# Optimization experiments

Hardware: AMD Instinct MI355X
Metric: run time of the kernel (lower is better)

Reference implementation:

```python
import jax, jax.numpy as jnp
import numpy as np

N_QUBITS = 10
Q_DEPTH = 6
MAX_LAYERS = 15
DIM = 2 ** N_QUBITS
INV_SQRT2 = 0.7071067811865476

# PennyLane ordering: wire 0 is the most-significant bit of the state index.
# All gates (H, RY, CNOT) are real, so the state stays real float32.

def _split(state, wire):
    a = 2 ** wire
    b = 2 ** (N_QUBITS - wire - 1)
    return state.reshape(-1, a, 2, b)

def apply_h(state, wire):
    s = _split(state, wire)
    s0, s1 = s[:, :, 0], s[:, :, 1]
    out = jnp.stack([(s0 + s1) * INV_SQRT2, (s0 - s1) * INV_SQRT2], axis=2)
    return out.reshape(-1, DIM)

def apply_ry(state, theta, wire):
    # theta: scalar (shared weight) or (B,) per-sample angle
    c = jnp.cos(theta * 0.5).reshape(-1, 1, 1)
    sn = jnp.sin(theta * 0.5).reshape(-1, 1, 1)
    s = _split(state, wire)
    s0, s1 = s[:, :, 0], s[:, :, 1]
    out = jnp.stack([c * s0 - sn * s1, sn * s0 + c * s1], axis=2)
    return out.reshape(-1, DIM)

def apply_cnot(state, ctrl):
    # CNOT on adjacent wires [ctrl, ctrl+1]
    a = 2 ** ctrl
    b = 2 ** (N_QUBITS - ctrl - 2)
    s = state.reshape(-1, a, 2, 2, b)
    out = jnp.stack([s[:, :, 0], s[:, :, 1, ::-1]], axis=2)
    return out.reshape(-1, DIM)

def expval_z(state):
    # <Z_j> = P(qubit j = 0) - P(qubit j = 1)
    zs = []
    for w in range(N_QUBITS):
        s = _split(state, w)
        p = s * s
        zs.append(jnp.sum(p[:, :, 0], axis=(1, 2)) - jnp.sum(p[:, :, 1], axis=(1, 2)))
    return jnp.stack(zs, axis=1)  # (B, n_qubits)

def simulate(q_in, q_params):
    B = q_in.shape[0]
    qw = q_params.reshape(MAX_LAYERS, N_QUBITS)
    state = jnp.zeros((B, DIM), q_in.dtype).at[:, 0].set(1.0)
    for w in range(N_QUBITS):
        state = apply_h(state, w)
    for w in range(N_QUBITS):
        state = apply_ry(state, q_in[:, w], w)
    for k in range(Q_DEPTH):
        for i in range(0, N_QUBITS - 1, 2):
            state = apply_cnot(state, i)
        for i in range(1, N_QUBITS - 1, 2):
            state = apply_cnot(state, i)
        for w in range(N_QUBITS):
            state = apply_ry(state, qw[k + 1, w], w)
    return expval_z(state)

def setup_inputs() -> dict:
    key = jax.random.key(0)
    k1, k2, k3, k4, k5 = jax.random.split(key, 5)
    B, D_IN, N_CLASSES = 8192, 512, 2
    return {
        "input_features": jax.random.normal(k1, (B, D_IN), jnp.float32),
        "W_red": jax.random.normal(k2, (N_QUBITS, D_IN), jnp.float32) * 0.04,
        "b_red": jnp.zeros((N_QUBITS,), jnp.float32),
        "q_params": 0.01 * jax.random.normal(k3, (MAX_LAYERS * N_QUBITS,), jnp.float32),
        "W_post": jax.random.normal(k4, (N_CLASSES, N_QUBITS), jnp.float32) * 0.3,
        "b_post": jax.random.normal(k5, (N_CLASSES,), jnp.float32) * 0.01,
    }

def reference(input_features, W_red, b_red, q_params, W_post, b_post):
    pre_out = input_features @ W_red.T + b_red           # (B, n_qubits)
    q_in = jnp.tanh(pre_out) * (np.pi / 2.0)             # angles in (-pi/2, pi/2)
    q_out = simulate(q_in, q_params)                     # (B, n_qubits) PauliZ expvals
    return q_out @ W_post.T + b_post                     # (B, n_classes)
```

## Files before the change

kernel.cpp:

```cpp
#include <hip/hip_runtime.h>
#include <math.h>

#define QDEPTH 6

typedef _Float16 h2 __attribute__((ext_vector_type(2)));

__device__ __forceinline__ int   h2i(h2 v)  { return __builtin_bit_cast(int, v); }
__device__ __forceinline__ h2    ih2(int v) { return __builtin_bit_cast(h2, v); }
__device__ __forceinline__ unsigned h2u(h2 v) { return __builtin_bit_cast(unsigned, v); }

__device__ __forceinline__ h2 cvt_pk(float a, float b) {
  return __builtin_bit_cast(h2, __builtin_amdgcn_cvt_pkrtz(a, b));
}

__device__ __forceinline__ h2 bper(int addr, h2 v) {
  return ih2(__builtin_amdgcn_ds_bpermute(addr, h2i(v)));
}

template<int CTRL>
__device__ __forceinline__ h2 dpph(h2 v) {
  int i = h2i(v);
  return ih2(__builtin_amdgcn_update_dpp(i, i, CTRL, 0xF, 0xF, true));
}

template<int CTRL>
__device__ __forceinline__ float dpp_add0(float v) {
  int i = __float_as_int(v);
  int r = __builtin_amdgcn_update_dpp(0, i, CTRL, 0xF, 0xF, false);
  return v + __int_as_float(r);
}

__device__ __forceinline__ float wave_sum(float v) {
  v = dpp_add0<0x111>(v);
  v = dpp_add0<0x112>(v);
  v = dpp_add0<0x114>(v);
  v = dpp_add0<0x118>(v);
  v = dpp_add0<0x142>(v);
  v = dpp_add0<0x143>(v);
  return v;
}

__device__ __forceinline__ float bcast63(float v) {
  return __int_as_float(__builtin_amdgcn_readlane(__float_as_int(v), 63));
}

__device__ __forceinline__ void pl32s(int& a, int& b) {
  asm("v_permlane32_swap_b32 %0, %1" : "+v"(a), "+v"(b));
}
__device__ __forceinline__ void pl16s(int& a, int& b) {
  asm("v_permlane16_swap_b32 %0, %1" : "+v"(a), "+v"(b));
}

__global__ void __launch_bounds__(256) qnet_kernel(
    const float* __restrict__ inp,
    const float* __restrict__ Wred,
    const float* __restrict__ bred,
    const float* __restrict__ qp,
    const float* __restrict__ Wpost,
    const float* __restrict__ bpost,
    float* __restrict__ out,
    int B) {
  __shared__ unsigned sco[QDEPTH * 29];
  {
    int t = threadIdx.x;
    if (t < 60) {
      int k = t / 10, w = t % 10;
      float ang = qp[(k + 1) * 10 + w] * 0.5f;
      float c = __cosf(ang), s = __sinf(ang);
      _Float16 ch = (_Float16)c, sh = (_Float16)s, nh = (_Float16)(-s);
      if (w < 9) {
        sco[k * 29 + w * 3 + 0] = h2u((h2){ch, ch});
        sco[k * 29 + w * 3 + 1] = h2u((h2){sh, sh});
        sco[k * 29 + w * 3 + 2] = h2u((h2){nh, nh});
      } else {
        sco[k * 29 + 27] = h2u((h2){ch, ch});
        sco[k * 29 + 28] = h2u((h2){nh, sh});
      }
    }
  }
  __syncthreads();

  int tid  = blockIdx.x * 256 + threadIdx.x;
  int wv   = tid >> 6;
  int lane = tid & 63;

  int o = lane ^ (((lane >> 4) & 1) << 3) ^ (((lane >> 2) & 1) << 1);
  int psrc = o ^ (((o >> 5) & 1) << 4) ^ (((o >> 3) & 1) << 2) ^ ((o >> 1) & 1);
  int addrP  = psrc << 2;
  int addrX4 = (lane ^ 4) << 2;
  bool cb1 = lane & 1;

  const float4* rA = (const float4*)(inp + (size_t)(2 * wv) * 512);
  const float4* rB = (const float4*)(inp + (size_t)(2 * wv + 1) * 512);
  float4 A0 = rA[lane], A1 = rA[lane + 64];
  float4 B0 = rB[lane], B1 = rB[lane + 64];
  float thA[10], thB[10];
#pragma unroll
  for (int q = 0; q < 10; ++q) {
    const float4* w4 = (const float4*)(Wred + q * 512);
    float4 w0 = w4[lane], w1 = w4[lane + 64];
    thA[q] = A0.x * w0.x + A0.y * w0.y + A0.z * w0.z + A0.w * w0.w
           + A1.x * w1.x + A1.y * w1.y + A1.z * w1.z + A1.w * w1.w;
    thB[q] = B0.x * w0.x + B0.y * w0.y + B0.z * w0.z + B0.w * w0.w
           + B1.x * w1.x + B1.y * w1.y + B1.z * w1.z + B1.w * w1.w;
  }

  h2 x[16];

#pragma unroll
  for (int e = 0; e < 2; ++e) {
    float g0[10], g1[10];
#pragma unroll
    for (int q = 0; q < 10; ++q) {
      float tot = bcast63(wave_sum(e ? thB[q] : thA[q])) + bred[q];
      float xc = fminf(fmaxf(tot, -15.f), 15.f);
      float u = __expf(2.f * xc);
      float tanhv = (u - 1.f) * __builtin_amdgcn_rcpf(u + 1.f);
      float t = tanhv * 0.78539816339744831f;
      float c = __cosf(t), s = __sinf(t);
      g0[q] = (c - s) * 0.70710678118654752f;
      g1[q] = (c + s) * 0.70710678118654752f;
    }
    float lf = 1.f;
#pragma unroll
    for (int w = 0; w < 6; ++w)
      lf *= ((lane >> (5 - w)) & 1) ? g1[w] : g0[w];
    float f67v[4];
#pragma unroll
    for (int j = 0; j < 4; ++j)
      f67v[j] = ((j & 2) ? g1[6] : g0[6]) * ((j & 1) ? g1[7] : g0[7]);
    float F89x[2], F89y[2];
    F89x[0] = g0[8] * g0[9]; F89y[0] = g0[8] * g1[9];
    F89x[1] = g1[8] * g0[9]; F89y[1] = g1[8] * g1[9];
#pragma unroll
    for (int i = 0; i < 8; ++i) {
      float m = lf * f67v[i >> 1];
      x[e * 8 + i] = cvt_pk(m * F89x[i & 1], m * F89y[i & 1]);
    }
  }

#pragma unroll
  for (int k = 0; k < QDEPTH; ++k) {
    const unsigned* L = sco + k * 29;

#pragma unroll
    for (int i = 0; i < 16; ++i) x[i] = bper(addrP, x[i]);
#pragma unroll
    for (int e = 0; e < 16; e += 8) {
      h2 t = x[e + 4]; x[e + 4] = x[e + 6]; x[e + 6] = t;
      t = x[e + 5]; x[e + 5] = x[e + 7]; x[e + 7] = t;
    }
#pragma unroll
    for (int e = 0; e < 16; e += 8) {
      h2 t = x[e + 2]; x[e + 2] = x[e + 3]; x[e + 3] = t;
      t = x[e + 6]; x[e + 6] = x[e + 7]; x[e + 7] = t;
    }

    { h2 cc9 = ih2(L[27]), ms9 = ih2(L[28]);
#pragma unroll
      for (int i = 0; i < 16; ++i) {
        h2 t = __builtin_shufflevector(x[i], x[i], 1, 0);
        int m = i & 7;
        bool flg = (m == 1 || m == 2 || m == 5 || m == 6);
        x[i] = flg ? (h2)(t * cc9 + x[i] * ms9) : (h2)(x[i] * cc9 + t * ms9);
      } }

    { h2 cc6 = ih2(L[18]), ss6 = ih2(L[19]), ns6 = ih2(L[20]);
      h2 AA = cb1 ? ns6 : cc6;
      h2 BB = cb1 ? cc6 : ns6;
      h2 CC = cb1 ? cc6 : ss6;
      h2 DD = cb1 ? ss6 : cc6;
#pragma unroll
      for (int i = 0; i < 16; ++i) if (!(i & 4)) {
        h2 u = x[i], w = x[i + 4];
        x[i]     = u * AA + w * BB;
        x[i + 4] = u * CC + w * DD;
      } }
    { h2 cc7 = ih2(L[21]), ss7 = ih2(L[22]), ns7 = ih2(L[23]);
#pragma unroll
      for (int i = 0; i < 16; ++i) if (!(i & 2)) {
        h2 u = x[i], w = x[i | 2];
        x[i]     = u * cc7 + w * ns7;
        x[i | 2] = w * cc7 + u * ss7;
      } }
    { h2 cc8 = ih2(L[24]), ss8 = ih2(L[25]), ns8 = ih2(L[26]);
#pragma unroll
      for (int i = 0; i < 16; ++i) if (!(i & 1)) {
        h2 u = x[i], w = x[i | 1];
        x[i]     = u * cc8 + w * ns8;
        x[i | 1] = w * cc8 + u * ss8;
      } }

    { h2 cc0 = ih2(L[0]), ss0 = ih2(L[1]), ns0 = ih2(L[2]);
#pragma unroll
      for (int j = 0; j < 8; ++j) {
        int a = h2i(x[2 * j]), b = h2i(x[2 * j + 1]);
        pl32s(a, b);
        h2 u = ih2(a), v = ih2(b);
        h2 nu = u * cc0 + v * ns0;
        h2 nv = v * cc0 + u * ss0;
        int na = h2i(nu), nb = h2i(nv);
        pl32s(na, nb);
        x[2 * j] = ih2(na); x[2 * j + 1] = ih2(nb);
      } }
    { h2 cc1 = ih2(L[3]), ss1 = ih2(L[4]), ns1 = ih2(L[5]);
#pragma unroll
      for (int j = 0; j < 8; ++j) {
        int a = h2i(x[2 * j]), b = h2i(x[2 * j + 1]);
        pl16s(a, b);
        h2 u = ih2(a), v = ih2(b);
        h2 nu = u * cc1 + v * ns1;
        h2 nv = v * cc1 + u * ss1;
        int na = h2i(nu), nb = h2i(nv);
        pl16s(na, nb);
        x[2 * j] = ih2(na); x[2 * j + 1] = ih2(nb);
      } }
    { h2 cc2 = ih2(L[6]), ss2 = ih2(L[7]), ns2 = ih2(L[8]);
      h2 gg = (lane & 8) ? ss2 : ns2;
#pragma unroll
      for (int i = 0; i < 16; ++i) {
        h2 p = dpph<0x128>(x[i]);
        x[i] = x[i] * cc2 + p * gg;
      } }
    { h2 cc3 = ih2(L[9]), ss3 = ih2(L[10]), ns3 = ih2(L[11]);
      h2 gg = (lane & 4) ? ss3 : ns3;
#pragma unroll
      for (int i = 0; i < 16; ++i) {
        h2 p = bper(addrX4, x[i]);
        x[i] = x[i] * cc3 + p * gg;
      } }
    { h2 cc4 = ih2(L[12]), ss4 = ih2(L[13]), ns4 = ih2(L[14]);
      h2 gg = (lane & 2) ? ss4 : ns4;
#pragma unroll
      for (int i = 0; i < 16; ++i) {
        h2 p = dpph<0x4E>(x[i]);
        x[i] = x[i] * cc4 + p * gg;
      } }
    { h2 cc5 = ih2(L[15]), ss5 = ih2(L[16]), ns5 = ih2(L[17]);
      h2 gg = (lane & 1) ? ss5 : ns5;
#pragma unroll
      for (int i = 0; i < 16; ++i) {
        h2 p = dpph<0xB1>(x[i]);
        x[i] = x[i] * cc5 + p * gg;
      } }
  }

  float A0w = 0.f, A1w = 0.f;
#pragma unroll
  for (int w = 0; w < 6; ++w) {
    bool b = (lane >> (5 - w)) & 1;
    A0w += b ? -Wpost[w] : Wpost[w];
    A1w += b ? -Wpost[10 + w] : Wpost[10 + w];
  }
  float oo[4];
#pragma unroll
  for (int e = 0; e < 2; ++e) {
    float q[8], d9 = 0.f;
#pragma unroll
    for (int i = 0; i < 8; ++i) {
      float lo = (float)x[e * 8 + i].x, hi = (float)x[e * 8 + i].y;
      float a2 = lo * lo, b2 = hi * hi;
      q[i] = a2 + b2;
      d9 += a2 - b2;
    }
    float A = q[0] + q[1], Bq = q[2] + q[3], C = q[4] + q[5], D = q[6] + q[7];
    float S  = (A + Bq) + (C + D);
    float z6 = (A + Bq) - (C + D);
    float z7 = (A - Bq) + (C - D);
    float E = q[0] - q[1], F = q[2] - q[3], G = q[4] - q[5], H = q[6] - q[7];
    float z8 = (E + F) + (G + H);
    float o0 = A0w * S + Wpost[6] * z6 + Wpost[7] * z7 + Wpost[8] * z8 + Wpost[9] * d9;
    float o1 = A1w * S + Wpost[16] * z6 + Wpost[17] * z7 + Wpost[18] * z8 + Wpost[19] * d9;
    oo[2 * e]     = wave_sum(o0);
    oo[2 * e + 1] = wave_sum(o1);
  }
  if (lane == 63) {
    float4 ov = { oo[0] + bpost[0], oo[1] + bpost[1],
                  oo[2] + bpost[0], oo[3] + bpost[1] };
    *(float4*)(out + 4 * (size_t)wv) = ov;
  }
}

extern "C" void kernel_launch(void* const* d_in, const int* in_sizes, int n_in,
                              void* d_out, int out_size, void* d_ws, size_t ws_size,
                              hipStream_t stream) {
  const float* inp   = (const float*)d_in[0];
  const float* Wred  = (const float*)d_in[1];
  const float* bred  = (const float*)d_in[2];
  const float* qp    = (const float*)d_in[3];
  const float* Wpost = (const float*)d_in[4];
  const float* bpost = (const float*)d_in[5];
  float* out = (float*)d_out;

  int B = in_sizes[0] / 512;
  int blocks = (B * 32) / 256;
  qnet_kernel<<<blocks, 256, 0, stream>>>(inp, Wred, bred, qp, Wpost, bpost, out, B);
}
```

Measured before the change: 99.02 us.

## Recast circuit as unitary matrix build plus MFMA GEMM on product states

The fixed entangling layers are now precomputed into a 1024x1024 fp16 unitary by simulating each basis state in a build kernel. A second kernel stores each sample's product-state factors (per-lane and per-register parts), and a third runs an MFMA GEMM that applies the unitary, squares the amplitudes, weights them by precomputed Z-sign-combined post weights and atomically accumulates into the output. This replaces per-sample shuffle-heavy gate simulation with dense matrix work. In exchange it performs far more FLOPs, needs three launches and workspace traffic, and relies on atomics and fp16 accumulation of the unitary.

```diff
diff --git a/kernel.cpp b/kernel.cpp
--- a/kernel.cpp
+++ b/kernel.cpp
@@ -4,14 +4,13 @@
 #define QDEPTH 6
 
 typedef _Float16 h2 __attribute__((ext_vector_type(2)));
+typedef _Float16 v8h __attribute__((ext_vector_type(8)));
+typedef float    v4f __attribute__((ext_vector_type(4)));
+typedef unsigned uu4 __attribute__((ext_vector_type(4)));
 
 __device__ __forceinline__ int   h2i(h2 v)  { return __builtin_bit_cast(int, v); }
 __device__ __forceinline__ h2    ih2(int v) { return __builtin_bit_cast(h2, v); }
 __device__ __forceinline__ unsigned h2u(h2 v) { return __builtin_bit_cast(unsigned, v); }
-
-__device__ __forceinline__ h2 cvt_pk(float a, float b) {
-  return __builtin_bit_cast(h2, __builtin_amdgcn_cvt_pkrtz(a, b));
-}
 
 __device__ __forceinline__ h2 bper(int addr, h2 v) {
   return ih2(__builtin_amdgcn_ds_bpermute(addr, h2i(v)));
@@ -51,44 +50,178 @@
   asm("v_permlane16_swap_b32 %0, %1" : "+v"(a), "+v"(b));
 }
 
-__global__ void __launch_bounds__(256) qnet_kernel(
-    const float* __restrict__ inp,
-    const float* __restrict__ Wred,
-    const float* __restrict__ bred,
-    const float* __restrict__ qp,
-    const float* __restrict__ Wpost,
-    const float* __restrict__ bpost,
-    float* __restrict__ out,
-    int B) {
+__device__ __forceinline__ void apply_layers(h2 (&x)[8], const unsigned* sco,
+                                             int lane, int addrP, int addrX4,
+                                             bool cb1) {
+  for (int k = 0; k < QDEPTH; ++k) {
+    const unsigned* L = sco + k * 29;
+#pragma unroll
+    for (int i = 0; i < 8; ++i) x[i] = bper(addrP, x[i]);
+    { h2 t = x[4]; x[4] = x[6]; x[6] = t; t = x[5]; x[5] = x[7]; x[7] = t; }
+    { h2 t = x[2]; x[2] = x[3]; x[3] = t; t = x[6]; x[6] = x[7]; x[7] = t; }
+    { h2 cc9 = ih2(L[27]), ms9 = ih2(L[28]);
+#pragma unroll
+      for (int i = 0; i < 8; ++i) {
+        h2 t = __builtin_shufflevector(x[i], x[i], 1, 0);
+        bool flg = (i == 1 || i == 2 || i == 5 || i == 6);
+        x[i] = flg ? (h2)(t * cc9 + x[i] * ms9) : (h2)(x[i] * cc9 + t * ms9);
+      } }
+    { h2 cc6 = ih2(L[18]), ss6 = ih2(L[19]), ns6 = ih2(L[20]);
+      h2 AA = cb1 ? ns6 : cc6;
+      h2 BB = cb1 ? cc6 : ns6;
+      h2 CC = cb1 ? cc6 : ss6;
+      h2 DD = cb1 ? ss6 : cc6;
+#pragma unroll
+      for (int i = 0; i < 4; ++i) {
+        h2 u = x[i], w = x[i + 4];
+        x[i]     = u * AA + w * BB;
+        x[i + 4] = u * CC + w * DD;
+      } }
+    { h2 cc7 = ih2(L[21]), ss7 = ih2(L[22]), ns7 = ih2(L[23]);
+#pragma unroll
+      for (int i = 0; i < 8; ++i) if (!(i & 2)) {
+        h2 u = x[i], w = x[i | 2];
+        x[i]     = u * cc7 + w * ns7;
+        x[i | 2] = w * cc7 + u * ss7;
+      } }
+    { h2 cc8 = ih2(L[24]), ss8 = ih2(L[25]), ns8 = ih2(L[26]);
+#pragma unroll
+      for (int i = 0; i < 8; ++i) if (!(i & 1)) {
+        h2 u = x[i], w = x[i | 1];
+        x[i]     = u * cc8 + w * ns8;
+        x[i | 1] = w * cc8 + u * ss8;
+      } }
+    { h2 cc0 = ih2(L[0]), ss0 = ih2(L[1]), ns0 = ih2(L[2]);
+#pragma unroll
+      for (int j = 0; j < 4; ++j) {
+        int a = h2i(x[2 * j]), b = h2i(x[2 * j + 1]);
+        pl32s(a, b);
+        h2 u = ih2(a), v = ih2(b);
+        h2 nu = u * cc0 + v * ns0;
+        h2 nv = v * cc0 + u * ss0;
+        int na = h2i(nu), nb = h2i(nv);
+        pl32s(na, nb);
+        x[2 * j] = ih2(na); x[2 * j + 1] = ih2(nb);
+      } }
+    { h2 cc1 = ih2(L[3]), ss1 = ih2(L[4]), ns1 = ih2(L[5]);
+#pragma unroll
+      for (int j = 0; j < 4; ++j) {
+        int a = h2i(x[2 * j]), b = h2i(x[2 * j + 1]);
+        pl16s(a, b);
+        h2 u = ih2(a), v = ih2(b);
+        h2 nu = u * cc1 + v * ns1;
+        h2 nv = v * cc1 + u * ss1;
+        int na = h2i(nu), nb = h2i(nv);
+        pl16s(na, nb);
+        x[2 * j] = ih2(na); x[2 * j + 1] = ih2(nb);
+      } }
+    { h2 cc2 = ih2(L[6]), ss2 = ih2(L[7]), ns2 = ih2(L[8]);
+      h2 gg = (lane & 8) ? ss2 : ns2;
+#pragma unroll
+      for (int i = 0; i < 8; ++i) {
+        h2 p = dpph<0x128>(x[i]);
+        x[i] = x[i] * cc2 + p * gg;
+      } }
+    { h2 cc3 = ih2(L[9]), ss3 = ih2(L[10]), ns3 = ih2(L[11]);
+      h2 gg = (lane & 4) ? ss3 : ns3;
+#pragma unroll
+      for (int i = 0; i < 8; ++i) {
+        h2 p = bper(addrX4, x[i]);
+        x[i] = x[i] * cc3 + p * gg;
+      } }
+    { h2 cc4 = ih2(L[12]), ss4 = ih2(L[13]), ns4 = ih2(L[14]);
+      h2 gg = (lane & 2) ? ss4 : ns4;
+#pragma unroll
+      for (int i = 0; i < 8; ++i) {
+        h2 p = dpph<0x4E>(x[i]);
+        x[i] = x[i] * cc4 + p * gg;
+      } }
+    { h2 cc5 = ih2(L[15]), ss5 = ih2(L[16]), ns5 = ih2(L[17]);
+      h2 gg = (lane & 1) ? ss5 : ns5;
+#pragma unroll
+      for (int i = 0; i < 8; ++i) {
+        h2 p = dpph<0xB1>(x[i]);
+        x[i] = x[i] * cc5 + p * gg;
+      } }
+  }
+}
+
+__device__ __forceinline__ void fill_sco(const float* qp, unsigned* sco) {
+  int t = threadIdx.x;
+  if (t < 60) {
+    int k = t / 10, w = t % 10;
+    float ang = qp[(k + 1) * 10 + w] * 0.5f;
+    float c = __cosf(ang), s = __sinf(ang);
+    _Float16 ch = (_Float16)c, sh = (_Float16)s, nh = (_Float16)(-s);
+    if (w < 9) {
+      sco[k * 29 + w * 3 + 0] = h2u((h2){ch, ch});
+      sco[k * 29 + w * 3 + 1] = h2u((h2){sh, sh});
+      sco[k * 29 + w * 3 + 2] = h2u((h2){nh, nh});
+    } else {
+      sco[k * 29 + 27] = h2u((h2){ch, ch});
+      sco[k * 29 + 28] = h2u((h2){nh, sh});
+    }
+  }
+}
+
+__global__ void __launch_bounds__(256) build_kernel(
+    const float* __restrict__ qp, const float* __restrict__ Wpost,
+    unsigned short* __restrict__ Bswz, float* __restrict__ w0,
+    float* __restrict__ w1) {
   __shared__ unsigned sco[QDEPTH * 29];
-  {
-    int t = threadIdx.x;
-    if (t < 60) {
-      int k = t / 10, w = t % 10;
-      float ang = qp[(k + 1) * 10 + w] * 0.5f;
-      float c = __cosf(ang), s = __sinf(ang);
-      _Float16 ch = (_Float16)c, sh = (_Float16)s, nh = (_Float16)(-s);
-      if (w < 9) {
-        sco[k * 29 + w * 3 + 0] = h2u((h2){ch, ch});
-        sco[k * 29 + w * 3 + 1] = h2u((h2){sh, sh});
-        sco[k * 29 + w * 3 + 2] = h2u((h2){nh, nh});
-      } else {
-        sco[k * 29 + 27] = h2u((h2){ch, ch});
-        sco[k * 29 + 28] = h2u((h2){nh, sh});
+  fill_sco(qp, sco);
+  __syncthreads();
+
+  int lane = threadIdx.x & 63;
+  int i = blockIdx.x * 4 + (threadIdx.x >> 6);
+
+  if (blockIdx.x == 0) {
+    for (int n = threadIdx.x; n < 1024; n += 256) {
+      float a0 = 0.f, a1 = 0.f;
+#pragma unroll
+      for (int w = 0; w < 10; ++w) {
+        float sg = ((n >> (9 - w)) & 1) ? -1.f : 1.f;
+        a0 += sg * Wpost[w];
+        a1 += sg * Wpost[10 + w];
       }
-    }
-  }
-  __syncthreads();
-
+      w0[n] = a0; w1[n] = a1;
+    }
+  }
+
+  int o = lane ^ (((lane >> 4) & 1) << 3) ^ (((lane >> 2) & 1) << 1);
+  int psrc = o ^ (((o >> 5) & 1) << 4) ^ (((o >> 3) & 1) << 2) ^ ((o >> 1) & 1);
+  int addrP = psrc << 2, addrX4 = (lane ^ 4) << 2;
+  bool cb1 = lane & 1;
+
+  h2 x[8];
+#pragma unroll
+  for (int r = 0; r < 8; ++r) {
+    int base = lane * 16 + 2 * r;
+    x[r] = (h2){ (_Float16)(base == i ? 1.f : 0.f),
+                 (_Float16)(base + 1 == i ? 1.f : 0.f) };
+  }
+
+  apply_layers(x, sco, lane, addrP, addrX4, cb1);
+
+  int kt = i >> 5, kk = i & 31;
+  int jj = kk & 7, hi16 = (kk >> 3) << 4;
+  size_t tbase = ((size_t)(lane * 32 + kt)) << 9;
+#pragma unroll
+  for (int r = 0; r < 8; ++r) {
+    unsigned u = h2u(x[r]);
+    Bswz[tbase + (size_t)((hi16 | (2 * r)) * 8 + jj)]     = (unsigned short)(u & 0xFFFF);
+    Bswz[tbase + (size_t)((hi16 | (2 * r + 1)) * 8 + jj)] = (unsigned short)(u >> 16);
+  }
+}
+
+__global__ void __launch_bounds__(256) glgr_kernel(
+    const float* __restrict__ inp, const float* __restrict__ Wred,
+    const float* __restrict__ bred, const float* __restrict__ bpost,
+    unsigned short* __restrict__ glane, unsigned short* __restrict__ greg,
+    float* __restrict__ out) {
   int tid  = blockIdx.x * 256 + threadIdx.x;
   int wv   = tid >> 6;
   int lane = tid & 63;
-
-  int o = lane ^ (((lane >> 4) & 1) << 3) ^ (((lane >> 2) & 1) << 1);
-  int psrc = o ^ (((o >> 5) & 1) << 4) ^ (((o >> 3) & 1) << 2) ^ ((o >> 1) & 1);
-  int addrP  = psrc << 2;
-  int addrX4 = (lane ^ 4) << 2;
-  bool cb1 = lane & 1;
 
   const float4* rA = (const float4*)(inp + (size_t)(2 * wv) * 512);
   const float4* rB = (const float4*)(inp + (size_t)(2 * wv + 1) * 512);
@@ -98,17 +231,16 @@
 #pragma unroll
   for (int q = 0; q < 10; ++q) {
     const float4* w4 = (const float4*)(Wred + q * 512);
-    float4 w0 = w4[lane], w1 = w4[lane + 64];
-    thA[q] = A0.x * w0.x + A0.y * w0.y + A0.z * w0.z + A0.w * w0.w
-           + A1.x * w1.x + A1.y * w1.y + A1.z * w1.z + A1.w * w1.w;
-    thB[q] = B0.x * w0.x + B0.y * w0.y + B0.z * w0.z + B0.w * w0.w
-           + B1.x * w1.x + B1.y * w1.y + B1.z * w1.z + B1.w * w1.w;
-  }
-
-  h2 x[16];
+    float4 w0v = w4[lane], w1v = w4[lane + 64];
+    thA[q] = A0.x * w0v.x + A0.y * w0v.y + A0.z * w0v.z + A0.w * w0v.w
+           + A1.x * w1v.x + A1.y * w1v.y + A1.z * w1v.z + A1.w * w1v.w;
+    thB[q] = B0.x * w0v.x + B0.y * w0v.y + B0.z * w0v.z + B0.w * w0v.w
+           + B1.x * w1v.x + B1.y * w1v.y + B1.z * w1v.z + B1.w * w1v.w;
+  }
 
 #pragma unroll
   for (int e = 0; e < 2; ++e) {
+    int el = 2 * wv + e;
     float g0[10], g1[10];
 #pragma unroll
     for (int q = 0; q < 10; ++q) {
@@ -125,159 +257,113 @@
 #pragma unroll
     for (int w = 0; w < 6; ++w)
       lf *= ((lane >> (5 - w)) & 1) ? g1[w] : g0[w];
-    float f67v[4];
-#pragma unroll
-    for (int j = 0; j < 4; ++j)
-      f67v[j] = ((j & 2) ? g1[6] : g0[6]) * ((j & 1) ? g1[7] : g0[7]);
-    float F89x[2], F89y[2];
-    F89x[0] = g0[8] * g0[9]; F89y[0] = g0[8] * g1[9];
-    F89x[1] = g1[8] * g0[9]; F89y[1] = g1[8] * g1[9];
-#pragma unroll
-    for (int i = 0; i < 8; ++i) {
-      float m = lf * f67v[i >> 1];
-      x[e * 8 + i] = cvt_pk(m * F89x[i & 1], m * F89y[i & 1]);
-    }
-  }
-
-#pragma unroll
-  for (int k = 0; k < QDEPTH; ++k) {
-    const unsigned* L = sco + k * 29;
-
-#pragma unroll
-    for (int i = 0; i < 16; ++i) x[i] = bper(addrP, x[i]);
-#pragma unroll
-    for (int e = 0; e < 16; e += 8) {
-      h2 t = x[e + 4]; x[e + 4] = x[e + 6]; x[e + 6] = t;
-      t = x[e + 5]; x[e + 5] = x[e + 7]; x[e + 7] = t;
-    }
-#pragma unroll
-    for (int e = 0; e < 16; e += 8) {
-      h2 t = x[e + 2]; x[e + 2] = x[e + 3]; x[e + 3] = t;
-      t = x[e + 6]; x[e + 6] = x[e + 7]; x[e + 7] = t;
-    }
-
-    { h2 cc9 = ih2(L[27]), ms9 = ih2(L[28]);
-#pragma unroll
-      for (int i = 0; i < 16; ++i) {
-        h2 t = __builtin_shufflevector(x[i], x[i], 1, 0);
-        int m = i & 7;
-        bool flg = (m == 1 || m == 2 || m == 5 || m == 6);
-        x[i] = flg ? (h2)(t * cc9 + x[i] * ms9) : (h2)(x[i] * cc9 + t * ms9);
-      } }
-
-    { h2 cc6 = ih2(L[18]), ss6 = ih2(L[19]), ns6 = ih2(L[20]);
-      h2 AA = cb1 ? ns6 : cc6;
-      h2 BB = cb1 ? cc6 : ns6;
-      h2 CC = cb1 ? cc6 : ss6;
-      h2 DD = cb1 ? ss6 : cc6;
-#pragma unroll
-      for (int i = 0; i < 16; ++i) if (!(i & 4)) {
-        h2 u = x[i], w = x[i + 4];
-        x[i]     = u * AA + w * BB;
-        x[i + 4] = u * CC + w * DD;
-      } }
-    { h2 cc7 = ih2(L[21]), ss7 = ih2(L[22]), ns7 = ih2(L[23]);
-#pragma unroll
-      for (int i = 0; i < 16; ++i) if (!(i & 2)) {
-        h2 u = x[i], w = x[i | 2];
-        x[i]     = u * cc7 + w * ns7;
-        x[i | 2] = w * cc7 + u * ss7;
-      } }
-    { h2 cc8 = ih2(L[24]), ss8 = ih2(L[25]), ns8 = ih2(L[26]);
-#pragma unroll
-      for (int i = 0; i < 16; ++i) if (!(i & 1)) {
-        h2 u = x[i], w = x[i | 1];
-        x[i]     = u * cc8 + w * ns8;
-        x[i | 1] = w * cc8 + u * ss8;
-      } }
-
-    { h2 cc0 = ih2(L[0]), ss0 = ih2(L[1]), ns0 = ih2(L[2]);
-#pragma unroll
-      for (int j = 0; j < 8; ++j) {
-        int a = h2i(x[2 * j]), b = h2i(x[2 * j + 1]);
-        pl32s(a, b);
-        h2 u = ih2(a), v = ih2(b);
-        h2 nu = u * cc0 + v * ns0;
-        h2 nv = v * cc0 + u * ss0;
-        int na = h2i(nu), nb = h2i(nv);
-        pl32s(na, nb);
-        x[2 * j] = ih2(na); x[2 * j + 1] = ih2(nb);
-      } }
-    { h2 cc1 = ih2(L[3]), ss1 = ih2(L[4]), ns1 = ih2(L[5]);
-#pragma unroll
-      for (int j = 0; j < 8; ++j) {
-        int a = h2i(x[2 * j]), b = h2i(x[2 * j + 1]);
-        pl16s(a, b);
-        h2 u = ih2(a), v = ih2(b);
-        h2 nu = u * cc1 + v * ns1;
-        h2 nv = v * cc1 + u * ss1;
-        int na = h2i(nu), nb = h2i(nv);
-        pl16s(na, nb);
-        x[2 * j] = ih2(na); x[2 * j + 1] = ih2(nb);
-      } }
-    { h2 cc2 = ih2(L[6]), ss2 = ih2(L[7]), ns2 = ih2(L[8]);
-      h2 gg = (lane & 8) ? ss2 : ns2;
-#pragma unroll
-      for (int i = 0; i < 16; ++i) {
-        h2 p = dpph<0x128>(x[i]);
-        x[i] = x[i] * cc2 + p * gg;
-      } }
-    { h2 cc3 = ih2(L[9]), ss3 = ih2(L[10]), ns3 = ih2(L[11]);
-      h2 gg = (lane & 4) ? ss3 : ns3;
-#pragma unroll
-      for (int i = 0; i < 16; ++i) {
-        h2 p = bper(addrX4, x[i]);
-        x[i] = x[i] * cc3 + p * gg;
-      } }
-    { h2 cc4 = ih2(L[12]), ss4 = ih2(L[13]), ns4 = ih2(L[14]);
-      h2 gg = (lane & 2) ? ss4 : ns4;
-#pragma unroll
-      for (int i = 0; i < 16; ++i) {
-        h2 p = dpph<0x4E>(x[i]);
-        x[i] = x[i] * cc4 + p * gg;
-      } }
-    { h2 cc5 = ih2(L[15]), ss5 = ih2(L[16]), ns5 = ih2(L[17]);
-      h2 gg = (lane & 1) ? ss5 : ns5;
-#pragma unroll
-      for (int i = 0; i < 16; ++i) {
-        h2 p = dpph<0xB1>(x[i]);
-        x[i] = x[i] * cc5 + p * gg;
-      } }
-  }
-
-  float A0w = 0.f, A1w = 0.f;
-#pragma unroll
-  for (int w = 0; w < 6; ++w) {
-    bool b = (lane >> (5 - w)) & 1;
-    A0w += b ? -Wpost[w] : Wpost[w];
-    A1w += b ? -Wpost[10 + w] : Wpost[10 + w];
-  }
-  float oo[4];
-#pragma unroll
-  for (int e = 0; e < 2; ++e) {
-    float q[8], d9 = 0.f;
-#pragma unroll
-    for (int i = 0; i < 8; ++i) {
-      float lo = (float)x[e * 8 + i].x, hi = (float)x[e * 8 + i].y;
-      float a2 = lo * lo, b2 = hi * hi;
-      q[i] = a2 + b2;
-      d9 += a2 - b2;
-    }
-    float A = q[0] + q[1], Bq = q[2] + q[3], C = q[4] + q[5], D = q[6] + q[7];
-    float S  = (A + Bq) + (C + D);
-    float z6 = (A + Bq) - (C + D);
-    float z7 = (A - Bq) + (C - D);
-    float E = q[0] - q[1], F = q[2] - q[3], G = q[4] - q[5], H = q[6] - q[7];
-    float z8 = (E + F) + (G + H);
-    float o0 = A0w * S + Wpost[6] * z6 + Wpost[7] * z7 + Wpost[8] * z8 + Wpost[9] * d9;
-    float o1 = A1w * S + Wpost[16] * z6 + Wpost[17] * z7 + Wpost[18] * z8 + Wpost[19] * d9;
-    oo[2 * e]     = wave_sum(o0);
-    oo[2 * e + 1] = wave_sum(o1);
-  }
-  if (lane == 63) {
-    float4 ov = { oo[0] + bpost[0], oo[1] + bpost[1],
-                  oo[2] + bpost[0], oo[3] + bpost[1] };
-    *(float4*)(out + 4 * (size_t)wv) = ov;
+    glane[(size_t)el * 64 + lane] =
+        (unsigned short)(h2u((h2){(_Float16)lf, (_Float16)lf}) & 0xFFFF);
+    if (lane < 16) {
+      int t4 = lane;
+      float gg = ((t4 & 8) ? g1[6] : g0[6]) * ((t4 & 4) ? g1[7] : g0[7])
+               * ((t4 & 2) ? g1[8] : g0[8]) * ((t4 & 1) ? g1[9] : g0[9]);
+      greg[(size_t)el * 16 + t4] =
+          (unsigned short)(h2u((h2){(_Float16)gg, (_Float16)gg}) & 0xFFFF);
+    }
+    if (lane == 0) {
+      out[2 * (size_t)el]     = bpost[0];
+      out[2 * (size_t)el + 1] = bpost[1];
+    }
+  }
+}
+
+__global__ void __launch_bounds__(256) gemm_kernel(
+    const unsigned short* __restrict__ Bswz,
+    const unsigned short* __restrict__ glane,
+    const unsigned short* __restrict__ greg,
+    const float* __restrict__ w0, const float* __restrict__ w1,
+    float* __restrict__ out) {
+  int bm = blockIdx.x >> 3, bn = blockIdx.x & 7;
+  int wvL  = threadIdx.x >> 6;
+  int lane = threadIdx.x & 63;
+  int wm = wvL >> 1, wn = wvL & 1;
+  int l15 = lane & 15, lhi = lane >> 4;
+  int rowBase = bm * 128 + wm * 64;
+  int hh = lhi & 1;
+  int gsel = lhi >> 1;
+
+  h2 grf[4][4];
+  int eA[4];
+#pragma unroll
+  for (int mt = 0; mt < 4; ++mt) {
+    eA[mt] = rowBase + mt * 16 + l15;
+    const uu4* gp = (const uu4*)(greg + (size_t)eA[mt] * 16 + hh * 8);
+    uu4 gu = *gp;
+    grf[mt][0] = ih2(gu.x); grf[mt][1] = ih2(gu.y);
+    grf[mt][2] = ih2(gu.z); grf[mt][3] = ih2(gu.w);
+  }
+
+  v4f acc[4][4];
+#pragma unroll
+  for (int mt = 0; mt < 4; ++mt)
+#pragma unroll
+    for (int nt = 0; nt < 4; ++nt) acc[mt][nt] = (v4f){0.f, 0.f, 0.f, 0.f};
+
+  int ntG0 = bn * 8 + wn * 4;
+
+#pragma unroll 2
+  for (int kt = 0; kt < 32; ++kt) {
+    v8h af[4];
+#pragma unroll
+    for (int mt = 0; mt < 4; ++mt) {
+      unsigned short gs = glane[(size_t)eA[mt] * 64 + kt * 2 + gsel];
+      h2 g2 = ih2((int)((unsigned)gs | ((unsigned)gs << 16)));
+      uu4 au;
+      au.x = h2u(g2 * grf[mt][0]);
+      au.y = h2u(g2 * grf[mt][1]);
+      au.z = h2u(g2 * grf[mt][2]);
+      au.w = h2u(g2 * grf[mt][3]);
+      af[mt] = __builtin_bit_cast(v8h, au);
+    }
+    v8h bf[4];
+#pragma unroll
+    for (int nt = 0; nt < 4; ++nt) {
+      const uu4* bp = (const uu4*)(Bswz + (((size_t)(ntG0 + nt) * 32 + kt) << 9)
+                                   + (size_t)lane * 8);
+      bf[nt] = __builtin_bit_cast(v8h, *bp);
+    }
+#pragma unroll
+    for (int mt = 0; mt < 4; ++mt)
+#pragma unroll
+      for (int nt = 0; nt < 4; ++nt)
+        acc[mt][nt] = __builtin_amdgcn_mfma_f32_16x16x32_f16(
+            af[mt], bf[nt], acc[mt][nt], 0, 0, 0);
+  }
+
+  float wa[4], wb[4];
+#pragma unroll
+  for (int nt = 0; nt < 4; ++nt) {
+    int n = bn * 128 + wn * 64 + nt * 16 + l15;
+    wa[nt] = w0[n]; wb[nt] = w1[n];
+  }
+#pragma unroll
+  for (int mt = 0; mt < 4; ++mt) {
+#pragma unroll
+    for (int j = 0; j < 4; ++j) {
+      float p0 = 0.f, p1 = 0.f;
+#pragma unroll
+      for (int nt = 0; nt < 4; ++nt) {
+        float c = acc[mt][nt][j];
+        float q = c * c;
+        p0 += q * wa[nt];
+        p1 += q * wb[nt];
+      }
+      p0 += __shfl_xor(p0, 1, 64); p1 += __shfl_xor(p1, 1, 64);
+      p0 += __shfl_xor(p0, 2, 64); p1 += __shfl_xor(p1, 2, 64);
+      p0 += __shfl_xor(p0, 4, 64); p1 += __shfl_xor(p1, 4, 64);
+      p0 += __shfl_xor(p0, 8, 64); p1 += __shfl_xor(p1, 8, 64);
+      if (l15 == 0) {
+        int e = rowBase + mt * 16 + lhi * 4 + j;
+        atomicAdd(&out[2 * (size_t)e],     p0);
+        atomicAdd(&out[2 * (size_t)e + 1], p1);
+      }
+    }
   }
 }
 
@@ -292,7 +378,16 @@
   const float* bpost = (const float*)d_in[5];
   float* out = (float*)d_out;
 
+  unsigned short* Bswz  = (unsigned short*)d_ws;
+  unsigned short* glane = (unsigned short*)((char*)d_ws + (2u << 20));
+  unsigned short* greg  = (unsigned short*)((char*)d_ws + (3u << 20));
+  float* w0 = (float*)((char*)d_ws + (3u << 20) + (256u << 10));
+  float* w1 = w0 + 1024;
+
   int B = in_sizes[0] / 512;
-  int blocks = (B * 32) / 256;
-  qnet_kernel<<<blocks, 256, 0, stream>>>(inp, Wred, bred, qp, Wpost, bpost, out, B);
-}
+
+  build_kernel<<<256, 256, 0, stream>>>(qp, Wpost, Bswz, w0, w1);
+  glgr_kernel<<<(B * 32) / 256, 256, 0, stream>>>(inp, Wred, bred, bpost,
+                                                  glane, greg, out);
+  gemm_kernel<<<(B / 128) * 8, 256, 0, stream>>>(Bswz, glane, greg, w0, w1, out);
+}
```

New measurement: 132.6 us. +34.0%, slower.
